# Optimization experiments

Hardware: AMD Instinct MI355X
Metric: run time of the kernel (lower is better)

The kernel has to match this reference:

```python
import jax, jax.numpy as jnp
import numpy as np

BANDS, ROWS, SIM_THRESH = 16, 8, 0.5


def setup_inputs() -> dict:
    key = jax.random.key(0)
    k1, k2 = jax.random.split(key)
    N, D = 8192, 256
    Z = jax.random.normal(k1, (N, D), dtype=jnp.float32)
    # random hyperplanes ~ N(0, I), (bands*rows, D) -- sampled once (torch samples in forward)
    planes = jax.random.normal(k2, (BANDS * ROWS, D), dtype=jnp.float32)
    return {"Z": Z, "planes": planes}


def reference(Z, planes):
    N, D = Z.shape
    # signature: sign of projections, (bands, rows, N); +/-1 vs bool is equivalent for bucketing
    sig_bits = (planes @ Z.T >= 0).reshape(BANDS, ROWS, N)
    # bit-pack each band's row-signature into an integer key == hashing the signature bytes
    bit_weights = (2 ** jnp.arange(ROWS)).astype(jnp.int32)
    keys = jnp.einsum('brn,r->bn', sig_bits.astype(jnp.int32), bit_weights)  # (bands, N)
    # cosine pairwise similarity (row-normalized GEMM)
    Zn = Z / jnp.linalg.norm(Z, axis=1, keepdims=True)
    sim = Zn @ Zn.T  # (N, N)
    # number of bands in which i and j fall in the same LSH bucket
    def band_match(acc, k):
        return acc + (k[:, None] == k[None, :]).astype(jnp.float32), None
    counts, _ = jax.lax.scan(band_match, jnp.zeros((N, N), jnp.float32), keys)
    # original masks the diagonal with -inf, thresholds at sim_thresh, and emits one
    # (sim) entry per matching band into an uncoalesced sparse tensor; densified this
    # is counts * sim on surviving off-diagonal pairs.
    mask = (sim >= SIM_THRESH) & (~jnp.eye(N, dtype=bool))
    return jnp.where(mask, counts * sim, 0.0)
```

## Files before the change

### kernel.cpp

```cpp
#include <hip/hip_runtime.h>

typedef __attribute__((ext_vector_type(8))) short short8;
typedef __attribute__((ext_vector_type(4))) float floatx4;

#define N_PTS 8192
#define D_DIM 256
#define N_PLANES 128

__device__ inline unsigned short f2bf(float f) {
    unsigned int x = __float_as_uint(f);
    unsigned int r = (x + 0x7fffu + ((x >> 16) & 1u)) >> 16;
    return (unsigned short)r;
}

__device__ inline int zbytes(unsigned int w) {
    unsigned int t = ((w & 0x7f7f7f7fu) + 0x7f7f7f7fu) | w | 0x7f7f7f7fu;
    return __popc(~t);
}

__device__ inline void load_lds16(const unsigned short* g, unsigned short* l) {
    __builtin_amdgcn_global_load_lds(
        (const __attribute__((address_space(1))) unsigned int*)g,
        (__attribute__((address_space(3))) unsigned int*)l, 16, 0, 0);
}

__global__ void norm_kernel(const float* __restrict__ Z,
                            unsigned short* __restrict__ Zn) {
    int n = blockIdx.x;
    int lane = threadIdx.x;
    const float4* zr = (const float4*)(Z + (size_t)n * D_DIM);
    float4 v = zr[lane];
    float ss = v.x * v.x + v.y * v.y + v.z * v.z + v.w * v.w;
#pragma unroll
    for (int off = 32; off > 0; off >>= 1) ss += __shfl_down(ss, off);
    ss = __shfl(ss, 0);
    float inv = rsqrtf(ss);
    ushort4 o;
    o.x = f2bf(v.x * inv);
    o.y = f2bf(v.y * inv);
    o.z = f2bf(v.z * inv);
    o.w = f2bf(v.w * inv);
    ((ushort4*)(Zn + (size_t)n * D_DIM))[lane] = o;
}

__global__ __launch_bounds__(256) void keys_kernel(
    const float* __restrict__ Z, const float* __restrict__ planes,
    unsigned int* __restrict__ keys4) {
    __shared__ __align__(16) float zs[16][D_DIM];
    int t = threadIdx.x;
    int base = blockIdx.x * 16;

    const float4* zsrc = (const float4*)(Z + (size_t)base * D_DIM);
    float4* zdst = (float4*)&zs[0][0];
#pragma unroll
    for (int i = 0; i < 4; ++i) zdst[t + i * 256] = zsrc[t + i * 256];
    __syncthreads();

    int p = t & 127;
    int hf = t >> 7;
    int wave = t >> 6, lane = t & 63;
    const float4* pr = (const float4*)(planes + (size_t)p * D_DIM);

    float acc[8] = {};
    for (int kk = 0; kk < D_DIM / 4; ++kk) {
        float4 pv = pr[kk];
#pragma unroll
        for (int j = 0; j < 8; ++j) {
            float4 zv = *(const float4*)&zs[hf * 8 + j][kk * 4];
            acc[j] += pv.x * zv.x + pv.y * zv.y + pv.z * zv.z + pv.w * zv.w;
        }
    }

#pragma unroll
    for (int j = 0; j < 8; ++j) {
        unsigned long long mask = __ballot(acc[j] >= 0.0f);
        if (lane < 2) {
            keys4[(size_t)(base + hf * 8 + j) * 4 + (wave & 1) * 2 + lane] =
                (unsigned int)(mask >> (32 * lane));
        }
    }
}

__global__ __launch_bounds__(256, 3) void gemm_kernel(
    const unsigned short* __restrict__ Zn, const uint4* __restrict__ keys,
    float* __restrict__ out) {
    __shared__ __align__(16) unsigned short stage[2048 * 8];
    __shared__ uint4 krow[128];
    __shared__ uint4 kcol[128];
    unsigned short* As = stage;
    unsigned short* Bs = stage + 8192;

    int t = threadIdx.x;
    int rowBase = blockIdx.y * 128;
    int colBase = blockIdx.x * 128;
    if (t < 128)
        krow[t] = keys[rowBase + t];
    else
        kcol[t - 128] = keys[colBase + (t - 128)];

    {
        float* tileOut = out + (size_t)rowBase * N_PTS + colBase;
        floatx4 z4 = {0.f, 0.f, 0.f, 0.f};
#pragma unroll
        for (int i = 0; i < 16; ++i) {
            int slot = i * 256 + t;
            int row = slot >> 5;
            int c4 = slot & 31;
            __builtin_nontemporal_store(
                z4, (floatx4*)(tileOut + (size_t)row * N_PTS + c4 * 4));
        }
    }

    int wave = t >> 6, lane = t & 63;
    int wm = wave >> 1, wn = wave & 1;
    int quad = lane >> 4, l16 = lane & 15;

    floatx4 acc[4][4] = {};

    for (int s = 0; s < 4; ++s) {
        __syncthreads();
#pragma unroll
        for (int i = 0; i < 4; ++i) {
            int sa = i * 256 + t;
            int c = sa >> 7, row = sa & 127;
            size_t gOff = (size_t)row * D_DIM + s * 64 + c * 8;
            load_lds16(Zn + (size_t)rowBase * D_DIM + gOff, &As[sa * 8]);
            load_lds16(Zn + (size_t)colBase * D_DIM + gOff, &Bs[sa * 8]);
        }
        __syncthreads();

#pragma unroll
        for (int k2 = 0; k2 < 2; ++k2) {
            int cb = k2 * 4 + quad;
            short8 afr[4], bfr[4];
#pragma unroll
            for (int mt = 0; mt < 4; ++mt)
                afr[mt] = *(const short8*)&As[(cb * 128 + wm * 64 + mt * 16 + l16) * 8];
#pragma unroll
            for (int nt = 0; nt < 4; ++nt)
                bfr[nt] = *(const short8*)&Bs[(cb * 128 + wn * 64 + nt * 16 + l16) * 8];
#pragma unroll
            for (int mt = 0; mt < 4; ++mt)
#pragma unroll
                for (int nt = 0; nt < 4; ++nt)
                    acc[mt][nt] = __builtin_amdgcn_mfma_f32_16x16x32_bf16(
                        afr[mt], bfr[nt], acc[mt][nt], 0, 0, 0);
        }
    }

#pragma unroll
    for (int mt = 0; mt < 4; ++mt) {
#pragma unroll
        for (int nt = 0; nt < 4; ++nt) {
            int lj = nt * 16 + l16;
            int gj = colBase + wn * 64 + lj;
            uint4 kj = kcol[wn * 64 + lj];
#pragma unroll
            for (int r = 0; r < 4; ++r) {
                int liL = wm * 64 + mt * 16 + quad * 4 + r;
                int gi = rowBase + liL;
                float s = acc[mt][nt][r];
                if (s >= 0.5f && gi != gj) {
                    uint4 ki = krow[liL];
                    int c = zbytes(ki.x ^ kj.x) + zbytes(ki.y ^ kj.y) +
                            zbytes(ki.z ^ kj.z) + zbytes(ki.w ^ kj.w);
                    out[(size_t)gi * N_PTS + gj] = s * (float)c;
                }
            }
        }
    }
}

extern "C" void kernel_launch(void* const* d_in, const int* in_sizes, int n_in,
                              void* d_out, int out_size, void* d_ws,
                              size_t ws_size, hipStream_t stream) {
    const float* Z = (const float*)d_in[0];
    const float* planes = (const float*)d_in[1];
    float* out = (float*)d_out;

    unsigned short* Zn = (unsigned short*)d_ws;
    unsigned int* keys4 =
        (unsigned int*)((char*)d_ws + (size_t)N_PTS * D_DIM * 2);

    norm_kernel<<<N_PTS, 64, 0, stream>>>(Z, Zn);
    keys_kernel<<<N_PTS / 16, 256, 0, stream>>>(Z, planes, keys4);
    gemm_kernel<<<dim3(N_PTS / 128, N_PTS / 128), 256, 0, stream>>>(
        Zn, (const uint4*)keys4, out);
}
```

Before: 328.4 us.

## Exploit symmetry with upper-triangular tiles and double-buffer LDS loads

The GEMM now runs only the upper-triangular 128x128 tile blocks, working out the tile coordinates from a linear block index. Each off-diagonal tile writes its result twice: a full nontemporal store to the upper tile, and a zero-fill plus scattered stores of nonzero values to the mirrored lower tile. This roughly halves the MFMA work and the operand loads. The LDS staging is also double-buffered so the next K-slice loads while the current one computes. The costs are uncoalesced transposed scatter stores, a larger LDS footprint with the occupancy hint removed, and a possible ordering race between the zero-fill and the mirrored stores, since different blocks touch the same lower tile.

Result: no change. 324.4 us (-1.2%).

```diff
diff --git a/kernel.cpp b/kernel.cpp
--- a/kernel.cpp
+++ b/kernel.cpp
@@ -6,6 +6,7 @@
 #define N_PTS 8192
 #define D_DIM 256
 #define N_PLANES 128
+#define NTILE 64
 
 __device__ inline unsigned short f2bf(float f) {
     unsigned int x = __float_as_uint(f);
@@ -81,25 +82,42 @@
     }
 }
 
-__global__ __launch_bounds__(256, 3) void gemm_kernel(
+__global__ __launch_bounds__(256) void gemm_kernel(
     const unsigned short* __restrict__ Zn, const uint4* __restrict__ keys,
     float* __restrict__ out) {
-    __shared__ __align__(16) unsigned short stage[2048 * 8];
+    __shared__ __align__(16) unsigned short As[2][8192];
+    __shared__ __align__(16) unsigned short Bs[2][8192];
     __shared__ uint4 krow[128];
     __shared__ uint4 kcol[128];
-    unsigned short* As = stage;
-    unsigned short* Bs = stage + 8192;
+
+    int idx = blockIdx.x;
+    int bi = (int)((129.0f - sqrtf(16641.0f - 8.0f * (float)idx)) * 0.5f);
+    while ((bi + 1) * NTILE - ((bi + 1) * bi) / 2 <= idx) ++bi;
+    while (bi * NTILE - (bi * (bi - 1)) / 2 > idx) --bi;
+    int bj = bi + (idx - (bi * NTILE - (bi * (bi - 1)) / 2));
+    int rowBase = bi * 128;
+    int colBase = bj * 128;
+    bool diag = (bi == bj);
 
     int t = threadIdx.x;
-    int rowBase = blockIdx.y * 128;
-    int colBase = blockIdx.x * 128;
     if (t < 128)
         krow[t] = keys[rowBase + t];
     else
         kcol[t - 128] = keys[colBase + (t - 128)];
 
-    {
-        float* tileOut = out + (size_t)rowBase * N_PTS + colBase;
+    const unsigned short* ZnA = Zn + (size_t)rowBase * D_DIM;
+    const unsigned short* ZnB = Zn + (size_t)colBase * D_DIM;
+#pragma unroll
+    for (int i = 0; i < 4; ++i) {
+        int sa = i * 256 + t;
+        int c = sa >> 7, row = sa & 127;
+        size_t gOff = (size_t)row * D_DIM + c * 8;
+        load_lds16(ZnA + gOff, &As[0][sa * 8]);
+        load_lds16(ZnB + gOff, &Bs[0][sa * 8]);
+    }
+
+    if (!diag) {
+        float* mOut = out + (size_t)colBase * N_PTS + rowBase;
         floatx4 z4 = {0.f, 0.f, 0.f, 0.f};
 #pragma unroll
         for (int i = 0; i < 16; ++i) {
@@ -107,7 +125,7 @@
             int row = slot >> 5;
             int c4 = slot & 31;
             __builtin_nontemporal_store(
-                z4, (floatx4*)(tileOut + (size_t)row * N_PTS + c4 * 4));
+                z4, (floatx4*)(mOut + (size_t)row * N_PTS + c4 * 4));
         }
     }
 
@@ -118,27 +136,29 @@
     floatx4 acc[4][4] = {};
 
     for (int s = 0; s < 4; ++s) {
+        int b = s & 1;
         __syncthreads();
-#pragma unroll
-        for (int i = 0; i < 4; ++i) {
-            int sa = i * 256 + t;
-            int c = sa >> 7, row = sa & 127;
-            size_t gOff = (size_t)row * D_DIM + s * 64 + c * 8;
-            load_lds16(Zn + (size_t)rowBase * D_DIM + gOff, &As[sa * 8]);
-            load_lds16(Zn + (size_t)colBase * D_DIM + gOff, &Bs[sa * 8]);
-        }
-        __syncthreads();
-
+        if (s < 3) {
+            int nb = b ^ 1;
+#pragma unroll
+            for (int i = 0; i < 4; ++i) {
+                int sa = i * 256 + t;
+                int c = sa >> 7, row = sa & 127;
+                size_t gOff = (size_t)row * D_DIM + (s + 1) * 64 + c * 8;
+                load_lds16(ZnA + gOff, &As[nb][sa * 8]);
+                load_lds16(ZnB + gOff, &Bs[nb][sa * 8]);
+            }
+        }
 #pragma unroll
         for (int k2 = 0; k2 < 2; ++k2) {
             int cb = k2 * 4 + quad;
             short8 afr[4], bfr[4];
 #pragma unroll
             for (int mt = 0; mt < 4; ++mt)
-                afr[mt] = *(const short8*)&As[(cb * 128 + wm * 64 + mt * 16 + l16) * 8];
+                afr[mt] = *(const short8*)&As[b][(cb * 128 + wm * 64 + mt * 16 + l16) * 8];
 #pragma unroll
             for (int nt = 0; nt < 4; ++nt)
-                bfr[nt] = *(const short8*)&Bs[(cb * 128 + wn * 64 + nt * 16 + l16) * 8];
+                bfr[nt] = *(const short8*)&Bs[b][(cb * 128 + wn * 64 + nt * 16 + l16) * 8];
 #pragma unroll
             for (int mt = 0; mt < 4; ++mt)
 #pragma unroll
@@ -160,12 +180,16 @@
                 int liL = wm * 64 + mt * 16 + quad * 4 + r;
                 int gi = rowBase + liL;
                 float s = acc[mt][nt][r];
+                float v = 0.0f;
                 if (s >= 0.5f && gi != gj) {
                     uint4 ki = krow[liL];
                     int c = zbytes(ki.x ^ kj.x) + zbytes(ki.y ^ kj.y) +
                             zbytes(ki.z ^ kj.z) + zbytes(ki.w ^ kj.w);
-                    out[(size_t)gi * N_PTS + gj] = s * (float)c;
+                    v = s * (float)c;
                 }
+                __builtin_nontemporal_store(v, out + (size_t)gi * N_PTS + gj);
+                if (v != 0.0f && !diag)
+                    out[(size_t)gj * N_PTS + gi] = v;
             }
         }
     }
@@ -184,6 +208,6 @@
 
     norm_kernel<<<N_PTS, 64, 0, stream>>>(Z, Zn);
     keys_kernel<<<N_PTS / 16, 256, 0, stream>>>(Z, planes, keys4);
-    gemm_kernel<<<dim3(N_PTS / 128, N_PTS / 128), 256, 0, stream>>>(
-        Zn, (const uint4*)keys4, out);
-}
+    int nblocks = NTILE * (NTILE + 1) / 2;
+    gemm_kernel<<<nblocks, 256, 0, stream>>>(Zn, (const uint4*)keys4, out);
+}
```
